# Optimization experiments

Hardware: AMD Instinct MI355X
Metric: run time of the kernel (lower is better)

The kernel has to match this reference:

```python
import math
import jax, jax.numpy as jnp
import numpy as np

N_HEADS = 12
D_EMBED = 768
BATCH = 2
SEQ = 2048


def setup_inputs() -> dict:
    key = jax.random.key(0)
    ks = jax.random.split(key, 5)
    scale = 0.02
    return {
        "x": jax.random.normal(ks[0], (BATCH, SEQ, D_EMBED), dtype=jnp.float32),
        "w_in": jax.random.normal(ks[1], (D_EMBED, 3 * D_EMBED), dtype=jnp.float32) * scale,
        "b_in": jax.random.normal(ks[2], (3 * D_EMBED,), dtype=jnp.float32) * scale,
        "w_out": jax.random.normal(ks[3], (D_EMBED, D_EMBED), dtype=jnp.float32) * scale,
        "b_out": jax.random.normal(ks[4], (D_EMBED,), dtype=jnp.float32) * scale,
    }


def reference(x, w_in, b_in, w_out, b_out):
    # x: [B, S, D]
    B, S, D = x.shape
    H = N_HEADS
    dh = D // H
    # Fused QKV projection: [B, S, 3D]
    qkv = x @ w_in + b_in
    q, k, v = jnp.split(qkv, 3, axis=-1)
    # [B, S, D] -> [B, H, S, dh]
    def to_heads(t):
        return t.reshape(B, S, H, dh).transpose(0, 2, 1, 3)
    q, k, v = to_heads(q), to_heads(k), to_heads(v)
    # Scaled dot-product attention (non-causal, masked=False default)
    scale = 1.0 / math.sqrt(dh)
    scores = jnp.einsum("bhqd,bhkd->bhqk", q, k) * scale  # [B, H, S, S]
    probs = jax.nn.softmax(scores, axis=-1)
    out = jnp.einsum("bhqk,bhkd->bhqd", probs, v)  # [B, H, S, dh]
    # Merge heads: [B, S, D]
    out = out.transpose(0, 2, 1, 3).reshape(B, S, D)
    return out @ w_out + b_out
```

## Files before the change

kernel.cpp:

```cpp
#include <hip/hip_runtime.h>
#include <stdint.h>

#define B_   2
#define S_   2048
#define D_   768
#define H_   12
#define DH_  64
#define N3_  2304
#define M_   4096

typedef __attribute__((ext_vector_type(8))) short   bf16x8;
typedef __attribute__((ext_vector_type(4))) float   f32x4;
typedef __attribute__((ext_vector_type(4))) int     i32x4;
typedef __attribute__((ext_vector_type(4))) unsigned short u16x4;

#define KSCALE 0.18033688011112042f

__device__ inline unsigned short f2bf(float f) {
    union { float f; unsigned u; } v; v.f = f;
    unsigned r = v.u + 0x7FFFu + ((v.u >> 16) & 1u);
    return (unsigned short)(r >> 16);
}

__device__ inline void async_copy16(const void* g, void* l) {
    __builtin_amdgcn_global_load_lds((const __attribute__((address_space(1))) void*)g,
                                     (__attribute__((address_space(3))) void*)l, 16, 0, 0);
}

__global__ void cvt_bf16(const float* __restrict__ in, unsigned short* __restrict__ out, int n4) {
    int i = blockIdx.x * blockDim.x + threadIdx.x;
    if (i >= n4) return;
    f32x4 v = *(const f32x4*)(in + (size_t)i * 4);
    u16x4 o;
    o.x = f2bf(v.x); o.y = f2bf(v.y); o.z = f2bf(v.z); o.w = f2bf(v.w);
    *(u16x4*)(out + (size_t)i * 4) = o;
}

__global__ void transpose_bf16(const float* __restrict__ in, unsigned short* __restrict__ out,
                               int R, int C) {
    __shared__ unsigned short t[32][33];
    int c0 = blockIdx.x * 32, r0 = blockIdx.y * 32;
    int tx = threadIdx.x, ty = threadIdx.y;
#pragma unroll
    for (int j = 0; j < 4; j++)
        t[ty + j * 8][tx] = f2bf(in[(size_t)(r0 + ty + j * 8) * C + c0 + tx]);
    __syncthreads();
#pragma unroll
    for (int j = 0; j < 4; j++)
        out[(size_t)(c0 + ty + j * 8) * R + r0 + tx] = t[tx][ty + j * 8];
}

__global__ void vtrans(const unsigned short* __restrict__ V, unsigned short* __restrict__ Vt) {
    __shared__ unsigned short t[64 * 65];
    const int bid = blockIdx.x;
    const int bh  = bid >> 5;
    const int s0  = (bid & 31) * 64;
    const int tid = threadIdx.x;
    const unsigned short* src = V  + (size_t)bh * S_ * DH_ + (size_t)s0 * DH_;
    unsigned short*       dst = Vt + (size_t)bh * DH_ * S_ + s0;
#pragma unroll
    for (int p = 0; p < 2; p++) {
        int c = p * 256 + tid;
        int s = c >> 3, dc = c & 7;
        i32x4 v = *(const i32x4*)&src[s * 64 + dc * 8];
        const unsigned short* e = (const unsigned short*)&v;
#pragma unroll
        for (int j = 0; j < 8; j++) t[(dc * 8 + j) * 65 + s] = e[j];
    }
    __syncthreads();
#pragma unroll
    for (int p = 0; p < 2; p++) {
        int c = p * 256 + tid;
        int d = c >> 3, sc = c & 7;
        unsigned short tmp[8];
#pragma unroll
        for (int j = 0; j < 8; j++) tmp[j] = t[d * 65 + sc * 8 + j];
        *(i32x4*)&dst[(size_t)d * S_ + sc * 8] = *(const i32x4*)tmp;
    }
}

template <int MODE>
__global__ __launch_bounds__(256) void gemm_bf16(
    const unsigned short* __restrict__ A,
    const unsigned short* __restrict__ Bt,
    const float* __restrict__ bias,
    void* __restrict__ Cout,
    unsigned short* __restrict__ Vnat,
    int M, int N, int K)
{
    __shared__ __align__(16) short Al[128 * 32];
    __shared__ __align__(16) short Bl[128 * 32];

    const int tid  = threadIdx.x;
    const int w    = tid >> 6;
    const int lane = tid & 63;
    const int r    = lane & 15;
    const int quad = lane >> 4;
    const int m0   = blockIdx.y * 128;
    const int n0   = blockIdx.x * 128;
    const int wm   = (w & 1) * 64;
    const int wn   = (w >> 1) * 64;

    f32x4 acc[4][4];
#pragma unroll
    for (int i = 0; i < 4; i++)
#pragma unroll
        for (int j = 0; j < 4; j++) acc[i][j] = f32x4{0.f, 0.f, 0.f, 0.f};

    const int c0 = tid, c1 = tid + 256;
    const size_t ga0 = (size_t)(m0 + (c0 >> 2)) * K + (c0 & 3) * 8;
    const size_t ga1 = (size_t)(m0 + (c1 >> 2)) * K + (c1 & 3) * 8;
    const size_t gb0 = (size_t)(n0 + (c0 >> 2)) * K + (c0 & 3) * 8;
    const size_t gb1 = (size_t)(n0 + (c1 >> 2)) * K + (c1 & 3) * 8;
    short* lA0 = &Al[(0 * 256 + w * 64) * 8];
    short* lA1 = &Al[(1 * 256 + w * 64) * 8];
    short* lB0 = &Bl[(0 * 256 + w * 64) * 8];
    short* lB1 = &Bl[(1 * 256 + w * 64) * 8];

    for (int k0 = 0; k0 < K; k0 += 32) {
        __syncthreads();
        async_copy16(A  + ga0 + k0, lA0);
        async_copy16(A  + ga1 + k0, lA1);
        async_copy16(Bt + gb0 + k0, lB0);
        async_copy16(Bt + gb1 + k0, lB1);
        __syncthreads();

        bf16x8 af[4], bf[4];
#pragma unroll
        for (int mi = 0; mi < 4; mi++)
            af[mi] = *(const bf16x8*)&Al[(wm + mi * 16 + r) * 32 + quad * 8];
#pragma unroll
        for (int ni = 0; ni < 4; ni++)
            bf[ni] = *(const bf16x8*)&Bl[(wn + ni * 16 + r) * 32 + quad * 8];
#pragma unroll
        for (int mi = 0; mi < 4; mi++)
#pragma unroll
            for (int ni = 0; ni < 4; ni++)
                acc[mi][ni] = __builtin_amdgcn_mfma_f32_16x16x32_bf16(
                    af[mi], bf[ni], acc[mi][ni], 0, 0, 0);
    }

    if (MODE == 0) {
        unsigned short* Q = (unsigned short*)Cout;
        const size_t one = (size_t)B_ * H_ * S_ * DH_;
#pragma unroll
        for (int ni = 0; ni < 4; ni++) {
            int col  = n0 + wn + ni * 16 + r;
            float bv = bias[col];
            int part = col / 768;
            int cc   = col - part * 768;
            int h    = cc >> 6;
            int d    = cc & 63;
            float scl = (part == 1) ? KSCALE : 1.0f;
            unsigned short* dst = (part == 2) ? Vnat : (Q + (size_t)part * one);
#pragma unroll
            for (int mi = 0; mi < 4; mi++) {
#pragma unroll
                for (int i = 0; i < 4; i++) {
                    int row = m0 + wm + mi * 16 + quad * 4 + i;
                    int b   = row >> 11;
                    int s   = row & 2047;
                    float v = (acc[mi][ni][i] + bv) * scl;
                    dst[(((size_t)(b * H_ + h)) * S_ + s) * DH_ + d] = f2bf(v);
                }
            }
        }
    } else {
        float* Cf = (float*)Cout;
#pragma unroll
        for (int ni = 0; ni < 4; ni++) {
            int col  = n0 + wn + ni * 16 + r;
            float bv = bias[col];
#pragma unroll
            for (int mi = 0; mi < 4; mi++) {
#pragma unroll
                for (int i = 0; i < 4; i++) {
                    int row = m0 + wm + mi * 16 + quad * 4 + i;
                    Cf[(size_t)row * N + col] = acc[mi][ni][i] + bv;
                }
            }
        }
    }
}

__global__ __launch_bounds__(256) void attn_kernel(
    const unsigned short* __restrict__ Q,
    const unsigned short* __restrict__ K,
    const unsigned short* __restrict__ Vt,
    unsigned short* __restrict__ Out)
{
    __shared__ __align__(16) short Kl[64 * 64];
    __shared__ __align__(16) short Vl[64 * 64];
    __shared__ __align__(16) short Pl[4][16 * 64];

    const int tid  = threadIdx.x;
    const int w    = tid >> 6;
    const int lane = tid & 63;
    const int r    = lane & 15;
    const int quad = lane >> 4;
    const int xk   = r & 7;
    const int bid  = blockIdx.x;
    const int bh   = bid % 24;
    const int qb   = bid / 24;
    const int b    = bh / H_;
    const int h    = bh - b * H_;
    const size_t baseQK = (size_t)bh * S_ * DH_;
    const size_t baseV  = (size_t)bh * DH_ * S_;
    const int q0   = qb * 64;

    bf16x8 qf[2];
    {
        const unsigned short* qp = Q + baseQK + (size_t)(q0 + w * 16 + r) * DH_ + quad * 8;
        qf[0] = *(const bf16x8*)(qp);
        qf[1] = *(const bf16x8*)(qp + 32);
    }

    f32x4 o[4];
#pragma unroll
    for (int nb = 0; nb < 4; nb++) o[nb] = f32x4{0.f, 0.f, 0.f, 0.f};
    float lsum[4] = {0.f, 0.f, 0.f, 0.f};

    const int srw = tid >> 3, schk = tid & 7;
    const unsigned short* kg = K  + baseQK + tid * 8;
    const unsigned short* vg = Vt + baseV + (size_t)srw * S_ + schk * 8;
    const int lb = srw * 64 + (schk ^ (srw & 7)) * 8;
    short* pl = &Pl[w][0];

    i32x4 kreg[2], vreg[2];
    kreg[0] = *(const i32x4*)(kg);
    kreg[1] = *(const i32x4*)(kg + 2048);
    vreg[0] = *(const i32x4*)(vg);
    vreg[1] = *(const i32x4*)(vg + 32 * S_);

    for (int kt = 0; kt < 32; kt++) {
        __syncthreads();
        *(i32x4*)&Kl[lb]        = kreg[0];
        *(i32x4*)&Kl[lb + 2048] = kreg[1];
        *(i32x4*)&Vl[lb]        = vreg[0];
        *(i32x4*)&Vl[lb + 2048] = vreg[1];
        __syncthreads();

        if (kt != 31) {
            const unsigned short* kn = kg + (kt + 1) * 4096;
            const unsigned short* vn = vg + (kt + 1) * 64;
            kreg[0] = *(const i32x4*)(kn);
            kreg[1] = *(const i32x4*)(kn + 2048);
            vreg[0] = *(const i32x4*)(vn);
            vreg[1] = *(const i32x4*)(vn + 32 * S_);
        }

        f32x4 sa[4];
#pragma unroll
        for (int nb = 0; nb < 4; nb++) sa[nb] = f32x4{0.f, 0.f, 0.f, 0.f};
#pragma unroll
        for (int t = 0; t < 2; t++)
#pragma unroll
            for (int nb = 0; nb < 4; nb++) {
                bf16x8 kf = *(const bf16x8*)&Kl[(nb * 16 + r) * 64 + ((t * 4 + quad) ^ xk) * 8];
                sa[nb] = __builtin_amdgcn_mfma_f32_16x16x32_bf16(qf[t], kf, sa[nb], 0, 0, 0);
            }

#pragma unroll
        for (int nb = 0; nb < 4; nb++)
#pragma unroll
            for (int i = 0; i < 4; i++) {
                float p = __builtin_amdgcn_exp2f(sa[nb][i]);
                lsum[i] += p;
                int prow = quad * 4 + i;
                int pch  = (nb * 2 + (r >> 3)) ^ (prow & 7);
                pl[prow * 64 + pch * 8 + (r & 7)] = (short)f2bf(p);
            }

        bf16x8 ap0 = *(const bf16x8*)&pl[r * 64 + ((0 * 4 + quad) ^ xk) * 8];
        bf16x8 ap1 = *(const bf16x8*)&pl[r * 64 + ((1 * 4 + quad) ^ xk) * 8];
#pragma unroll
        for (int nb = 0; nb < 4; nb++) {
            bf16x8 v0 = *(const bf16x8*)&Vl[(nb * 16 + r) * 64 + ((0 * 4 + quad) ^ xk) * 8];
            bf16x8 v1 = *(const bf16x8*)&Vl[(nb * 16 + r) * 64 + ((1 * 4 + quad) ^ xk) * 8];
            o[nb] = __builtin_amdgcn_mfma_f32_16x16x32_bf16(ap0, v0, o[nb], 0, 0, 0);
            o[nb] = __builtin_amdgcn_mfma_f32_16x16x32_bf16(ap1, v1, o[nb], 0, 0, 0);
        }
    }

#pragma unroll
    for (int i = 0; i < 4; i++) {
        float l = lsum[i];
        l += __shfl_xor(l, 1);
        l += __shfl_xor(l, 2);
        l += __shfl_xor(l, 4);
        l += __shfl_xor(l, 8);
        float inv = 1.0f / l;
        int s = q0 + w * 16 + quad * 4 + i;
        size_t ob = ((size_t)b * S_ + s) * D_ + h * DH_;
#pragma unroll
        for (int nb = 0; nb < 4; nb++)
            Out[ob + nb * 16 + r] = f2bf(o[nb][i] * inv);
    }
}

extern "C" void kernel_launch(void* const* d_in, const int* in_sizes, int n_in,
                              void* d_out, int out_size, void* d_ws, size_t ws_size,
                              hipStream_t stream) {
    const float* x     = (const float*)d_in[0];
    const float* w_in  = (const float*)d_in[1];
    const float* b_in  = (const float*)d_in[2];
    const float* w_out = (const float*)d_in[3];
    const float* b_out = (const float*)d_in[4];
    float* out = (float*)d_out;
    char* ws = (char*)d_ws;

    unsigned short* xb    = (unsigned short*)(ws);
    unsigned short* winT  = (unsigned short*)(ws + 6291456);
    unsigned short* woutT = (unsigned short*)(ws + 9830400);
    unsigned short* QKV   = (unsigned short*)(ws + 11010048);
    unsigned short* tmpV  = (unsigned short*)(ws + 29884416);

    const size_t one = (size_t)B_ * H_ * S_ * DH_;
    unsigned short* Vtbuf  = QKV + 2 * one;
    unsigned short* attnO  = xb;

    cvt_bf16<<<3072, 256, 0, stream>>>(x, xb, (M_ * D_) / 4);
    transpose_bf16<<<dim3(N3_ / 32, D_ / 32), dim3(32, 8), 0, stream>>>(w_in, winT, D_, N3_);
    transpose_bf16<<<dim3(D_ / 32, D_ / 32), dim3(32, 8), 0, stream>>>(w_out, woutT, D_, D_);

    gemm_bf16<0><<<dim3(N3_ / 128, M_ / 128), 256, 0, stream>>>(
        xb, winT, b_in, (void*)QKV, tmpV, M_, N3_, D_);

    vtrans<<<24 * 32, 256, 0, stream>>>(tmpV, Vtbuf);

    attn_kernel<<<B_ * H_ * (S_ / 64), 256, 0, stream>>>(
        QKV, QKV + one, Vtbuf, attnO);

    gemm_bf16<1><<<dim3(D_ / 128, M_ / 128), 256, 0, stream>>>(
        attnO, woutT, b_out, (void*)out, nullptr, M_, D_, D_);
}
```

Before: 183.4 us.

## Keep attention probabilities in registers via transposed S and fp16 PV MFMA

The attention kernel now computes S transposed (K as the A operand), so the exp'd probabilities land in the register layout the 16x16x16 fp16 MFMA expects for P·V. This removes the per-tile LDS round trip for P. Each wave now handles 32 query rows instead of 16, halving the grid and reusing each K/V LDS tile across two query tiles. V is stored as fp16 by the QKV GEMM epilogue, and row sums are computed with an MFMA against a ones vector instead of shuffles. The risks are fp16 range and precision for V and P (P uses round-toward-zero conversion), higher register pressure, and fewer blocks for occupancy.

```diff
diff --git a/kernel.cpp b/kernel.cpp
--- a/kernel.cpp
+++ b/kernel.cpp
@@ -9,10 +9,12 @@
 #define N3_  2304
 #define M_   4096
 
-typedef __attribute__((ext_vector_type(8))) short   bf16x8;
-typedef __attribute__((ext_vector_type(4))) float   f32x4;
-typedef __attribute__((ext_vector_type(4))) int     i32x4;
+typedef __attribute__((ext_vector_type(8))) short    bf16x8;
+typedef __attribute__((ext_vector_type(4))) float    f32x4;
+typedef __attribute__((ext_vector_type(4))) int      i32x4;
 typedef __attribute__((ext_vector_type(4))) unsigned short u16x4;
+typedef _Float16 f16x4 __attribute__((ext_vector_type(4)));
+typedef __fp16   h16x2 __attribute__((ext_vector_type(2)));
 
 #define KSCALE 0.18033688011112042f
 
@@ -161,7 +163,15 @@
                     int b   = row >> 11;
                     int s   = row & 2047;
                     float v = (acc[mi][ni][i] + bv) * scl;
-                    dst[(((size_t)(b * H_ + h)) * S_ + s) * DH_ + d] = f2bf(v);
+                    unsigned short bits;
+                    if (part == 2) {
+                        union { _Float16 h; unsigned short s; } cv;
+                        cv.h = (_Float16)v;
+                        bits = cv.s;
+                    } else {
+                        bits = f2bf(v);
+                    }
+                    dst[(((size_t)(b * H_ + h)) * S_ + s) * DH_ + d] = bits;
                 }
             }
         }
@@ -191,7 +201,6 @@
 {
     __shared__ __align__(16) short Kl[64 * 64];
     __shared__ __align__(16) short Vl[64 * 64];
-    __shared__ __align__(16) short Pl[4][16 * 64];
 
     const int tid  = threadIdx.x;
     const int w    = tid >> 6;
@@ -206,25 +215,32 @@
     const int h    = bh - b * H_;
     const size_t baseQK = (size_t)bh * S_ * DH_;
     const size_t baseV  = (size_t)bh * DH_ * S_;
-    const int q0   = qb * 64;
-
-    bf16x8 qf[2];
-    {
-        const unsigned short* qp = Q + baseQK + (size_t)(q0 + w * 16 + r) * DH_ + quad * 8;
-        qf[0] = *(const bf16x8*)(qp);
-        qf[1] = *(const bf16x8*)(qp + 32);
-    }
-
-    f32x4 o[4];
-#pragma unroll
-    for (int nb = 0; nb < 4; nb++) o[nb] = f32x4{0.f, 0.f, 0.f, 0.f};
-    float lsum[4] = {0.f, 0.f, 0.f, 0.f};
+    const int q0   = qb * 128;
+
+    bf16x8 qf[2][2];
+#pragma unroll
+    for (int qt = 0; qt < 2; qt++) {
+        const unsigned short* qp =
+            Q + baseQK + (size_t)(q0 + w * 32 + qt * 16 + r) * DH_ + quad * 8;
+        qf[qt][0] = *(const bf16x8*)(qp);
+        qf[qt][1] = *(const bf16x8*)(qp + 32);
+    }
+
+    f32x4 o[2][4];
+    f32x4 lacc[2];
+#pragma unroll
+    for (int qt = 0; qt < 2; qt++) {
+        lacc[qt] = f32x4{0.f, 0.f, 0.f, 0.f};
+#pragma unroll
+        for (int nb = 0; nb < 4; nb++) o[qt][nb] = f32x4{0.f, 0.f, 0.f, 0.f};
+    }
+
+    const f16x4 ONES = {(_Float16)1.f, (_Float16)1.f, (_Float16)1.f, (_Float16)1.f};
 
     const int srw = tid >> 3, schk = tid & 7;
     const unsigned short* kg = K  + baseQK + tid * 8;
     const unsigned short* vg = Vt + baseV + (size_t)srw * S_ + schk * 8;
     const int lb = srw * 64 + (schk ^ (srw & 7)) * 8;
-    short* pl = &Pl[w][0];
 
     i32x4 kreg[2], vreg[2];
     kreg[0] = *(const i32x4*)(kg);
@@ -249,53 +265,66 @@
             vreg[1] = *(const i32x4*)(vn + 32 * S_);
         }
 
-        f32x4 sa[4];
-#pragma unroll
-        for (int nb = 0; nb < 4; nb++) sa[nb] = f32x4{0.f, 0.f, 0.f, 0.f};
+        f32x4 sa[2][4];
+#pragma unroll
+        for (int qt = 0; qt < 2; qt++)
+#pragma unroll
+            for (int kb = 0; kb < 4; kb++) sa[qt][kb] = f32x4{0.f, 0.f, 0.f, 0.f};
 #pragma unroll
         for (int t = 0; t < 2; t++)
 #pragma unroll
+            for (int kb = 0; kb < 4; kb++) {
+                bf16x8 kf = *(const bf16x8*)&Kl[(kb * 16 + r) * 64 + ((t * 4 + quad) ^ xk) * 8];
+#pragma unroll
+                for (int qt = 0; qt < 2; qt++)
+                    sa[qt][kb] = __builtin_amdgcn_mfma_f32_16x16x32_bf16(
+                        kf, qf[qt][t], sa[qt][kb], 0, 0, 0);
+            }
+
+        f16x4 pf[2][4];
+#pragma unroll
+        for (int qt = 0; qt < 2; qt++)
+#pragma unroll
+            for (int kb = 0; kb < 4; kb++) {
+                float p0 = __builtin_amdgcn_exp2f(sa[qt][kb][0]);
+                float p1 = __builtin_amdgcn_exp2f(sa[qt][kb][1]);
+                float p2 = __builtin_amdgcn_exp2f(sa[qt][kb][2]);
+                float p3 = __builtin_amdgcn_exp2f(sa[qt][kb][3]);
+                union { f16x4 v; h16x2 h[2]; } u;
+                u.h[0] = __builtin_amdgcn_cvt_pkrtz(p0, p1);
+                u.h[1] = __builtin_amdgcn_cvt_pkrtz(p2, p3);
+                pf[qt][kb] = u.v;
+            }
+
+#pragma unroll
+        for (int kb = 0; kb < 4; kb++) {
+#pragma unroll
             for (int nb = 0; nb < 4; nb++) {
-                bf16x8 kf = *(const bf16x8*)&Kl[(nb * 16 + r) * 64 + ((t * 4 + quad) ^ xk) * 8];
-                sa[nb] = __builtin_amdgcn_mfma_f32_16x16x32_bf16(qf[t], kf, sa[nb], 0, 0, 0);
-            }
-
-#pragma unroll
-        for (int nb = 0; nb < 4; nb++)
-#pragma unroll
-            for (int i = 0; i < 4; i++) {
-                float p = __builtin_amdgcn_exp2f(sa[nb][i]);
-                lsum[i] += p;
-                int prow = quad * 4 + i;
-                int pch  = (nb * 2 + (r >> 3)) ^ (prow & 7);
-                pl[prow * 64 + pch * 8 + (r & 7)] = (short)f2bf(p);
-            }
-
-        bf16x8 ap0 = *(const bf16x8*)&pl[r * 64 + ((0 * 4 + quad) ^ xk) * 8];
-        bf16x8 ap1 = *(const bf16x8*)&pl[r * 64 + ((1 * 4 + quad) ^ xk) * 8];
-#pragma unroll
-        for (int nb = 0; nb < 4; nb++) {
-            bf16x8 v0 = *(const bf16x8*)&Vl[(nb * 16 + r) * 64 + ((0 * 4 + quad) ^ xk) * 8];
-            bf16x8 v1 = *(const bf16x8*)&Vl[(nb * 16 + r) * 64 + ((1 * 4 + quad) ^ xk) * 8];
-            o[nb] = __builtin_amdgcn_mfma_f32_16x16x32_bf16(ap0, v0, o[nb], 0, 0, 0);
-            o[nb] = __builtin_amdgcn_mfma_f32_16x16x32_bf16(ap1, v1, o[nb], 0, 0, 0);
-        }
-    }
-
-#pragma unroll
-    for (int i = 0; i < 4; i++) {
-        float l = lsum[i];
-        l += __shfl_xor(l, 1);
-        l += __shfl_xor(l, 2);
-        l += __shfl_xor(l, 4);
-        l += __shfl_xor(l, 8);
-        float inv = 1.0f / l;
-        int s = q0 + w * 16 + quad * 4 + i;
-        size_t ob = ((size_t)b * S_ + s) * D_ + h * DH_;
-#pragma unroll
-        for (int nb = 0; nb < 4; nb++)
-            Out[ob + nb * 16 + r] = f2bf(o[nb][i] * inv);
-    }
+                f16x4 vf = *(const f16x4*)&Vl[(nb * 16 + r) * 64 +
+                                              ((kb * 2 + (quad >> 1)) ^ xk) * 8 + (quad & 1) * 4];
+#pragma unroll
+                for (int qt = 0; qt < 2; qt++)
+                    o[qt][nb] = __builtin_amdgcn_mfma_f32_16x16x16f16(
+                        pf[qt][kb], vf, o[qt][nb], 0, 0, 0);
+            }
+#pragma unroll
+            for (int qt = 0; qt < 2; qt++)
+                lacc[qt] = __builtin_amdgcn_mfma_f32_16x16x16f16(
+                    pf[qt][kb], ONES, lacc[qt], 0, 0, 0);
+        }
+    }
+
+#pragma unroll
+    for (int qt = 0; qt < 2; qt++)
+#pragma unroll
+        for (int i = 0; i < 4; i++) {
+            float inv = 1.0f / lacc[qt][i];
+            int s = q0 + w * 32 + qt * 16 + quad * 4 + i;
+            size_t ob = ((size_t)b * S_ + s) * D_ + h * DH_;
+#pragma unroll
+            for (int nb = 0; nb < 4; nb++)
+                Out[ob + nb * 16 + r] = f2bf(o[qt][nb][i] * inv);
+        }
 }
 
 extern "C" void kernel_launch(void* const* d_in, const int* in_sizes, int n_in,
@@ -328,7 +357,7 @@
 
     vtrans<<<24 * 32, 256, 0, stream>>>(tmpV, Vtbuf);
 
-    attn_kernel<<<B_ * H_ * (S_ / 64), 256, 0, stream>>>(
+    attn_kernel<<<24 * (S_ / 128), 256, 0, stream>>>(
         QKV, QKV + one, Vtbuf, attnO);
 
     gemm_bf16<1><<<dim3(D_ / 128, M_ / 128), 256, 0, stream>>>(
```

After: 184.9 us. Within noise of the previous version (+0.9%).
